# Kernel optimization log

Measured on AMD Instinct MI355X. Metric: run time of the kernel, lower is better.

The kernel has to match this reference:

```python
import jax, jax.numpy as jnp
import numpy as np

B, I, H = 16384, 512, 512
HH = H // 2


def _lrelu(v):
    return jnp.where(v > 0, v, 0.01 * v)


def setup_inputs() -> dict:
    key = jax.random.key(0)
    ks = jax.random.split(key, 20)
    s = 1.0 / np.sqrt(H)
    rn = lambda k, shp, sc: (jax.random.normal(k, shp, jnp.float32) * sc)
    return {
        "x": rn(ks[0], (B, I), 1.0),
        "h0": rn(ks[1], (1, B, H), 1.0),
        "c0": rn(ks[2], (1, B, H), 1.0),
        "cum": jax.random.uniform(ks[3], (B, 1), jnp.float32),
        # LSTM params (torch gate order i, f, g, o)
        "W_ih": rn(ks[4], (4 * H, I), s),
        "W_hh": rn(ks[5], (4 * H, H), s),
        "b_ih": rn(ks[6], (4 * H,), s),
        "b_hh": rn(ks[7], (4 * H,), s),
        # skip gate MLP
        "W_sp": rn(ks[8], (HH, H), s),
        "b_sp": rn(ks[9], (HH,), s),
        "W_sc": rn(ks[10], (HH, H), s),
        "b_sc": rn(ks[11], (HH,), s),
        "W_so": rn(ks[12], (1, HH), s),
        "b_so": rn(ks[13], (1,), s),
        # threshold gate MLP
        "W_tp": rn(ks[14], (HH, H), s),
        "b_tp": rn(ks[15], (HH,), s),
        "W_to": rn(ks[16], (1, HH), s),
        "b_to": rn(ks[17], (1,), s),
    }


def reference(x, h0, c0, cum, W_ih, W_hh, b_ih, b_hh,
              W_sp, b_sp, W_sc, b_sc, W_so, b_so,
              W_tp, b_tp, W_to, b_to):
    # single-step, single-layer LSTM
    gates = x @ W_ih.T + b_ih + h0[0] @ W_hh.T + b_hh  # [B, 4H]
    i_g, f_g, g_g, o_g = jnp.split(gates, 4, axis=-1)
    i_g = jax.nn.sigmoid(i_g)
    f_g = jax.nn.sigmoid(f_g)
    g_g = jnp.tanh(g_g)
    o_g = jax.nn.sigmoid(o_g)
    c1l = f_g * c0[0] + i_g * g_g          # [B, H]
    h1l = o_g * jnp.tanh(c1l)              # [B, H]
    h1, c1 = h1l[None], c1l[None]          # [1, B, H]

    # skip gate: delta prob from c0[-1], c1[-1]
    sg = _lrelu(c0[-1] @ W_sp.T + b_sp + c1[-1] @ W_sc.T + b_sc)  # [B, H/2]
    update_prob_delta = jax.nn.sigmoid(sg @ W_so.T + b_so)        # [B, 1]

    # threshold gate from c0[-1]
    tg = _lrelu(c0[-1] @ W_tp.T + b_tp)                           # [B, H/2]
    update_threshold = jax.nn.sigmoid(tg @ W_to.T + b_to)         # [B, 1]

    update_prob = cum + jnp.minimum(update_prob_delta, 1.0 - cum)  # [B, 1]
    # straight-through round: fwd hard threshold, bwd identity to prob
    hard = (update_prob > update_threshold).astype(jnp.float32)
    update_gate = update_prob + jax.lax.stop_gradient(hard - update_prob)

    new_h = update_gate * h1 + (1.0 - update_gate) * h0  # [1, B, H]
    new_c = update_gate * c1 + (1.0 - update_gate) * c0  # [1, B, H]
    update_cum = (1.0 - update_gate) * update_prob        # [B, 1]
    return (new_h, new_c, update_cum, update_prob_delta, update_prob)
```

## Files before the change

kernel.cpp:

```cpp
#include <hip/hip_runtime.h>
#include <math.h>

#define BB 16384
#define HH 512

typedef short short8 __attribute__((ext_vector_type(8)));
typedef float f32x4 __attribute__((ext_vector_type(4)));
typedef unsigned short ushort_t;

__device__ __forceinline__ float sigm(float v){ return 1.0f/(1.0f+expf(-v)); }

__device__ __forceinline__ unsigned short f2bf(float f){
    unsigned int u = __float_as_uint(f);
    u = u + 0x7FFFu + ((u>>16)&1u);
    return (unsigned short)(u>>16);
}
__device__ __forceinline__ float bf2f(unsigned short h){
    return __uint_as_float(((unsigned int)h)<<16);
}
__device__ __forceinline__ void gll16(const void* g, void* l){
    __builtin_amdgcn_global_load_lds((const __attribute__((address_space(1))) void*)g,
                                     (__attribute__((address_space(3))) void*)l, 16, 0, 0);
}
__device__ __forceinline__ void split_store(float v, ushort_t* ph, ushort_t* pl, int j){
    unsigned short h = f2bf(v);
    unsigned short l = f2bf(v - bf2f(h));
    ph[j] = h; pl[j] = l;
}

__global__ void k_prep_all(
    const float* __restrict__ x, const float* __restrict__ h0, const float* __restrict__ c0,
    const float* __restrict__ W_ih, const float* __restrict__ W_hh,
    const float* __restrict__ b_ih, const float* __restrict__ b_hh,
    const float* __restrict__ W_sp, const float* __restrict__ W_sc, const float* __restrict__ W_tp,
    const float* __restrict__ b_sp, const float* __restrict__ b_sc, const float* __restrict__ b_tp,
    ushort_t* __restrict__ A1h, ushort_t* __restrict__ A1l,
    ushort_t* __restrict__ A2h, ushort_t* __restrict__ A2l,
    ushort_t* __restrict__ B1h, ushort_t* __restrict__ B1l,
    ushort_t* __restrict__ B2h, ushort_t* __restrict__ B2l,
    float* __restrict__ bgp, float* __restrict__ bs2)
{
    int bid = blockIdx.x;
    if (bid < 8192) {
        int u = bid*256 + threadIdx.x;
        int r  = u & 255;
        int c  = (u >> 8) & 3;
        int kt = (u >> 10) & 31;
        int tm = u >> 15;
        int row = tm*256 + r;
        int k0 = kt*32 + c*8;
        const float* src = (k0 < 512) ? (x + (size_t)row*512 + k0)
                                      : (h0 + (size_t)row*512 + (k0-512));
        float4 v0 = *(const float4*)(src);
        float4 v1 = *(const float4*)(src+4);
        float vv[8] = {v0.x,v0.y,v0.z,v0.w,v1.x,v1.y,v1.z,v1.w};
        size_t off = (size_t)u * 8;
#pragma unroll
        for (int j=0;j<8;++j) split_store(vv[j], A1h+off, A1l+off, j);
    } else if (bid < 12288) {
        int u = (bid-8192)*256 + threadIdx.x;
        int r  = u & 127;
        int c  = (u >> 7) & 3;
        int tk = (u >> 9) & 15;
        int tm = u >> 13;
        int row = tm*128 + r;
        int k0 = tk*32 + c*8;
        const float* src = c0 + (size_t)row*512 + k0;
        float4 v0 = *(const float4*)(src);
        float4 v1 = *(const float4*)(src+4);
        float vv[8] = {v0.x,v0.y,v0.z,v0.w,v1.x,v1.y,v1.z,v1.w};
        size_t off = ((size_t)tm*32 + tk)*4096 + (size_t)(c*128 + r)*8;
#pragma unroll
        for (int j=0;j<8;++j) split_store(vv[j], A2h+off, A2l+off, j);
    } else if (bid < 13312) {
        int u = (bid-12288)*256 + threadIdx.x;
        int r  = u & 255;
        int c  = (u >> 8) & 3;
        int kt = (u >> 10) & 31;
        int tn = u >> 15;
        int g = (r>>4)&3;
        int h = tn*64 + (r>>6)*16 + (r&15);
        int wrow = g*512 + h;
        int k0 = kt*32 + c*8;
        const float* src = (k0 < 512) ? (W_ih + (size_t)wrow*512 + k0)
                                      : (W_hh + (size_t)wrow*512 + (k0-512));
        float4 v0 = *(const float4*)(src);
        float4 v1 = *(const float4*)(src+4);
        float vv[8] = {v0.x,v0.y,v0.z,v0.w,v1.x,v1.y,v1.z,v1.w};
        size_t off = (size_t)u * 8;
#pragma unroll
        for (int j=0;j<8;++j) split_store(vv[j], B1h+off, B1l+off, j);
        if (kt == 0 && c == 0) bgp[tn*256 + r] = b_ih[wrow] + b_hh[wrow];
    } else {
        int u = (bid-13312)*256 + threadIdx.x;
        int r  = u & 127;
        int c  = (u >> 7) & 3;
        int tk = (u >> 9) & 31;
        int tn = u >> 14;
        int n = tn*128 + r;
        int k0 = tk*32 + c*8;
        float vv[8];
        if (n < 256) {
            const float* src = (k0 < 512) ? (W_sp + (size_t)n*512 + k0)
                                          : (W_sc + (size_t)n*512 + (k0-512));
            float4 v0 = *(const float4*)(src);
            float4 v1 = *(const float4*)(src+4);
            vv[0]=v0.x; vv[1]=v0.y; vv[2]=v0.z; vv[3]=v0.w;
            vv[4]=v1.x; vv[5]=v1.y; vv[6]=v1.z; vv[7]=v1.w;
        } else if (k0 < 512) {
            const float* src = W_tp + (size_t)(n-256)*512 + k0;
            float4 v0 = *(const float4*)(src);
            float4 v1 = *(const float4*)(src+4);
            vv[0]=v0.x; vv[1]=v0.y; vv[2]=v0.z; vv[3]=v0.w;
            vv[4]=v1.x; vv[5]=v1.y; vv[6]=v1.z; vv[7]=v1.w;
        } else {
#pragma unroll
            for (int j=0;j<8;++j) vv[j] = 0.0f;
        }
        size_t off = (size_t)u * 8;
#pragma unroll
        for (int j=0;j<8;++j) split_store(vv[j], B2h+off, B2l+off, j);
        if (tk == 0 && c == 0) bs2[n] = (n < 256) ? (b_sp[n] + b_sc[n]) : b_tp[n-256];
    }
}

#define GSTEP(T, CA, CB, NA, NB, DO_READS, DO_STAGE, VMASM)                          \
  {                                                                                  \
    if (DO_READS) {                                                                  \
        const ushort_t* bufA1 = &lds[((T)+1) & 3][0];                                \
        const ushort_t* bufB1 = &lds[((T)+1) & 3][8192];                             \
        _Pragma("unroll") for (int f = 0; f < 8; ++f)                                \
            NA[f] = *(const short8*)&bufA1[aoff[f]];                                 \
        _Pragma("unroll") for (int f = 0; f < 4; ++f)                                \
            NB[f] = *(const short8*)&bufB1[boff[f]];                                 \
    }                                                                                \
    if (DO_STAGE) {                                                                  \
        const int uu = (T) + 3;                                                      \
        const ushort_t* As_ = ((uu >> 5) == 1) ? Al : Ah;                            \
        const ushort_t* Bs_ = ((uu >> 5) == 2) ? Bl : Bh;                            \
        size_t ga = ((size_t)tm*32 + (uu & 31))*8192 + (size_t)tid*8;                \
        size_t gb = ((size_t)tn*32 + (uu & 31))*8192 + (size_t)tid*8;                \
        ushort_t* dA = &lds[uu & 3][0];                                              \
        ushort_t* dB = &lds[uu & 3][8192];                                           \
        gll16(As_ + ga,        dA + tid*8);                                          \
        gll16(As_ + ga + 4096, dA + 4096 + tid*8);                                   \
        gll16(Bs_ + gb,        dB + tid*8);                                          \
        gll16(Bs_ + gb + 4096, dB + 4096 + tid*8);                                   \
    }                                                                                \
    _Pragma("unroll") for (int fm = 0; fm < 8; ++fm)                                 \
        _Pragma("unroll") for (int fn = 0; fn < 4; ++fn)                             \
            acc[fm][fn] = __builtin_amdgcn_mfma_f32_16x16x32_bf16(CA[fm], CB[fn], acc[fm][fn], 0,0,0); \
    VMASM;                                                                           \
    asm volatile("s_barrier" ::: "memory");                                          \
  }

__global__ __launch_bounds__(512, 2) void k_gemm_gates(
    const ushort_t* __restrict__ Ah, const ushort_t* __restrict__ Al,
    const ushort_t* __restrict__ Bh, const ushort_t* __restrict__ Bl,
    const float* __restrict__ bgp, const float* __restrict__ c0,
    float* __restrict__ outH, float* __restrict__ outC,
    ushort_t* __restrict__ A2h, ushort_t* __restrict__ A2l)
{
    __shared__ __align__(16) ushort_t lds[4][16384];
    const int tid  = threadIdx.x;
    const int lane = tid & 63;
    const int wid  = tid >> 6;
    const int wr   = wid >> 2;
    const int wc   = wid & 3;
    const int l15  = lane & 15;
    const int lq   = lane >> 4;
    const int bid  = (int)blockIdx.x;
    const int v    = (bid & 7)*64 + (bid >> 3);
    const int tm   = v >> 3;
    const int tn   = v & 7;

    f32x4 acc[8][4];
#pragma unroll
    for (int fn = 0; fn < 4; ++fn) {
        float bv = bgp[tn*256 + wc*64 + fn*16 + l15];
#pragma unroll
        for (int fm = 0; fm < 8; ++fm) {
            acc[fm][fn][0]=bv; acc[fm][fn][1]=bv; acc[fm][fn][2]=bv; acc[fm][fn][3]=bv;
        }
    }

    int aoff[8], boff[4];
#pragma unroll
    for (int f = 0; f < 8; ++f) aoff[f] = (lq*256 + wr*128 + f*16 + l15) * 8;
#pragma unroll
    for (int f = 0; f < 4; ++f) boff[f] = (lq*256 + wc*64 + f*16 + l15) * 8;

    short8 a0[8], b0[4], a1[8], b1[4];

#pragma unroll
    for (int u0 = 0; u0 < 3; ++u0) {
        size_t ga = ((size_t)tm*32 + u0)*8192 + (size_t)tid*8;
        size_t gb = ((size_t)tn*32 + u0)*8192 + (size_t)tid*8;
        gll16(Ah + ga,        &lds[u0][0]     + tid*8);
        gll16(Ah + ga + 4096, &lds[u0][4096]  + tid*8);
        gll16(Bh + gb,        &lds[u0][8192]  + tid*8);
        gll16(Bh + gb + 4096, &lds[u0][12288] + tid*8);
    }
    asm volatile("s_waitcnt vmcnt(4)" ::: "memory");
    asm volatile("s_barrier" ::: "memory");
#pragma unroll
    for (int f = 0; f < 8; ++f) a0[f] = *(const short8*)&lds[0][aoff[f]];
#pragma unroll
    for (int f = 0; f < 4; ++f) b0[f] = *(const short8*)&lds[0][8192 + boff[f]];

    for (int t = 0; t < 92; t += 2) {
        GSTEP(t,   a0, b0, a1, b1, 1, 1, asm volatile("s_waitcnt vmcnt(4)" ::: "memory"));
        GSTEP(t+1, a1, b1, a0, b0, 1, 1, asm volatile("s_waitcnt vmcnt(4)" ::: "memory"));
    }
    GSTEP(92, a0, b0, a1, b1, 1, 1, asm volatile("s_waitcnt vmcnt(4)" ::: "memory"));
    GSTEP(93, a1, b1, a0, b0, 1, 0, asm volatile("s_waitcnt vmcnt(0)" ::: "memory"));
    GSTEP(94, a0, b0, a1, b1, 1, 0, ((void)0));
    GSTEP(95, a1, b1, a0, b0, 0, 0, ((void)0));

    const int h = tn*64 + wc*16 + l15;
#pragma unroll
    for (int fm = 0; fm < 8; ++fm) {
        int row0 = tm*256 + wr*128 + fm*16 + lq*4;
#pragma unroll
        for (int r = 0; r < 4; ++r) {
            int row = row0 + r;
            size_t idx = (size_t)row*512 + h;
            float ig = sigm(acc[fm][0][r]);
            float fg = sigm(acc[fm][1][r]);
            float gg = tanhf(acc[fm][2][r]);
            float og = sigm(acc[fm][3][r]);
            float c1 = fg*c0[idx] + ig*gg;
            float h1 = og*tanhf(c1);
            outC[idx] = c1;
            outH[idx] = h1;
            unsigned short ch = f2bf(c1);
            unsigned short cl = f2bf(c1 - bf2f(ch));
            size_t a2 = ((size_t)(row>>7)*32 + 16 + (h>>5))*4096
                      + (size_t)((((h>>3)&3))*128 + (row&127))*8 + (h&7);
            A2h[a2] = ch;
            A2l[a2] = cl;
        }
    }
}

#define SSTEP(T, CA, CB, NA, NB, DO_READS, DO_STAGE, VMASM)                          \
  {                                                                                  \
    if (DO_READS) {                                                                  \
        const ushort_t* bufA1 = &lds2[((T)+1) & 3][0];                               \
        const ushort_t* bufB1 = &lds2[((T)+1) & 3][4096];                            \
        _Pragma("unroll") for (int f = 0; f < 4; ++f)                                \
            NA[f] = *(const short8*)&bufA1[aoff[f]];                                 \
        _Pragma("unroll") for (int f = 0; f < 4; ++f)                                \
            NB[f] = *(const short8*)&bufB1[boff[f]];                                 \
    }                                                                                \
    if (DO_STAGE) {                                                                  \
        const int uu = (T) + 3;                                                      \
        const ushort_t* As_ = ((uu >> 5) == 1) ? Al : Ah;                            \
        const ushort_t* Bs_ = ((uu >> 5) == 2) ? Bl : Bh;                            \
        size_t ga = ((size_t)tm*32 + (uu & 31))*4096 + (size_t)tid*8;                \
        size_t gb = ((size_t)tn*32 + (uu & 31))*4096 + (size_t)tid*8;                \
        ushort_t* dA = &lds2[uu & 3][0];                                             \
        ushort_t* dB = &lds2[uu & 3][4096];                                          \
        gll16(As_ + ga,        dA + tid*8);                                          \
        gll16(As_ + ga + 2048, dA + 2048 + tid*8);                                   \
        gll16(Bs_ + gb,        dB + tid*8);                                          \
        gll16(Bs_ + gb + 2048, dB + 2048 + tid*8);                                   \
    }                                                                                \
    _Pragma("unroll") for (int fm = 0; fm < 4; ++fm)                                 \
        _Pragma("unroll") for (int fn = 0; fn < 4; ++fn)                             \
            acc[fm][fn] = __builtin_amdgcn_mfma_f32_16x16x32_bf16(CA[fm], CB[fn], acc[fm][fn], 0,0,0); \
    VMASM;                                                                           \
    asm volatile("s_barrier" ::: "memory");                                          \
  }

__global__ __launch_bounds__(256, 2) void k_gemm_sgtg(
    const ushort_t* __restrict__ Ah, const ushort_t* __restrict__ Al,
    const ushort_t* __restrict__ Bh, const ushort_t* __restrict__ Bl,
    const float* __restrict__ bs2,
    float* __restrict__ sgtg)
{
    __shared__ __align__(16) ushort_t lds2[4][8192];
    const int tid  = threadIdx.x;
    const int lane = tid & 63;
    const int wid  = tid >> 6;
    const int wr   = wid >> 1;
    const int wc   = wid & 1;
    const int l15  = lane & 15;
    const int lq   = lane >> 4;
    const int bid  = (int)blockIdx.x;
    const int v    = (bid & 7)*64 + (bid >> 3);
    const int tm   = v >> 2;
    const int tn   = v & 3;

    f32x4 acc[4][4];
#pragma unroll
    for (int fn = 0; fn < 4; ++fn) {
        float bv = bs2[tn*128 + wc*64 + fn*16 + l15];
#pragma unroll
        for (int fm = 0; fm < 4; ++fm) {
            acc[fm][fn][0]=bv; acc[fm][fn][1]=bv; acc[fm][fn][2]=bv; acc[fm][fn][3]=bv;
        }
    }

    int aoff[4], boff[4];
#pragma unroll
    for (int f = 0; f < 4; ++f) {
        aoff[f] = (lq*128 + wr*64 + f*16 + l15) * 8;
        boff[f] = (lq*128 + wc*64 + f*16 + l15) * 8;
    }

    short8 a0[4], b0[4], a1[4], b1[4];

#pragma unroll
    for (int u0 = 0; u0 < 3; ++u0) {
        size_t ga = ((size_t)tm*32 + u0)*4096 + (size_t)tid*8;
        size_t gb = ((size_t)tn*32 + u0)*4096 + (size_t)tid*8;
        gll16(Ah + ga,        &lds2[u0][0]    + tid*8);
        gll16(Ah + ga + 2048, &lds2[u0][2048] + tid*8);
        gll16(Bh + gb,        &lds2[u0][4096] + tid*8);
        gll16(Bh + gb + 2048, &lds2[u0][6144] + tid*8);
    }
    asm volatile("s_waitcnt vmcnt(4)" ::: "memory");
    asm volatile("s_barrier" ::: "memory");
#pragma unroll
    for (int f = 0; f < 4; ++f) a0[f] = *(const short8*)&lds2[0][aoff[f]];
#pragma unroll
    for (int f = 0; f < 4; ++f) b0[f] = *(const short8*)&lds2[0][4096 + boff[f]];

    for (int t = 0; t < 92; t += 2) {
        SSTEP(t,   a0, b0, a1, b1, 1, 1, asm volatile("s_waitcnt vmcnt(4)" ::: "memory"));
        SSTEP(t+1, a1, b1, a0, b0, 1, 1, asm volatile("s_waitcnt vmcnt(4)" ::: "memory"));
    }
    SSTEP(92, a0, b0, a1, b1, 1, 1, asm volatile("s_waitcnt vmcnt(4)" ::: "memory"));
    SSTEP(93, a1, b1, a0, b0, 1, 0, asm volatile("s_waitcnt vmcnt(0)" ::: "memory"));
    SSTEP(94, a0, b0, a1, b1, 1, 0, ((void)0));
    SSTEP(95, a1, b1, a0, b0, 0, 0, ((void)0));

#pragma unroll
    for (int fm = 0; fm < 4; ++fm) {
        int row0 = tm*128 + wr*64 + fm*16 + lq*4;
#pragma unroll
        for (int fn = 0; fn < 4; ++fn) {
            int n = tn*128 + wc*64 + fn*16 + l15;
#pragma unroll
            for (int r = 0; r < 4; ++r) {
                int row = row0 + r;
                float vv = acc[fm][fn][r];
                vv = vv > 0.f ? vv : 0.01f*vv;
                sgtg[(size_t)row*512 + n] = vv;
            }
        }
    }
}

__global__ __launch_bounds__(256) void k_final(
    const float* __restrict__ sgtg,
    const float* __restrict__ h0, const float* __restrict__ c0,
    const float* __restrict__ cum,
    const float* __restrict__ W_so, const float* __restrict__ b_so,
    const float* __restrict__ W_to, const float* __restrict__ b_to,
    float* __restrict__ outH, float* __restrict__ outC,
    float* __restrict__ outCum, float* __restrict__ outDelta, float* __restrict__ outProb)
{
    int w = threadIdx.x >> 6;
    int lane = threadIdx.x & 63;
    int b = blockIdx.x * 4 + w;
    const float* row = sgtg + (size_t)b * 512;
    float so = 0.f, to = 0.f;
#pragma unroll
    for (int u = 0; u < 4; ++u) {
        int c = lane + 64 * u;
        so = fmaf(row[c], W_so[c], so);
        to = fmaf(row[256 + c], W_to[c], to);
    }
#pragma unroll
    for (int off = 32; off; off >>= 1) {
        so += __shfl_down(so, off);
        to += __shfl_down(to, off);
    }
    so = __shfl(so, 0);
    to = __shfl(to, 0);
    float delta = sigm(so + b_so[0]);
    float thr   = sigm(to + b_to[0]);
    float cu = cum[b];
    float prob = cu + fminf(delta, 1.0f - cu);
    float hard = (prob > thr) ? 1.0f : 0.0f;
    if (lane == 0) {
        outDelta[b] = delta;
        outProb[b]  = prob;
        outCum[b]   = (1.0f - hard) * prob;
    }
    if (hard == 0.0f) {
#pragma unroll
        for (int u = 0; u < 8; ++u) {
            size_t idx = (size_t)b * 512 + lane + 64 * u;
            outH[idx] = h0[idx];
            outC[idx] = c0[idx];
        }
    }
}

extern "C" void kernel_launch(void* const* d_in, const int* in_sizes, int n_in,
                              void* d_out, int out_size, void* d_ws, size_t ws_size,
                              hipStream_t stream)
{
    const float* x    = (const float*)d_in[0];
    const float* h0   = (const float*)d_in[1];
    const float* c0   = (const float*)d_in[2];
    const float* cum  = (const float*)d_in[3];
    const float* W_ih = (const float*)d_in[4];
    const float* W_hh = (const float*)d_in[5];
    const float* b_ih = (const float*)d_in[6];
    const float* b_hh = (const float*)d_in[7];
    const float* W_sp = (const float*)d_in[8];
    const float* b_sp = (const float*)d_in[9];
    const float* W_sc = (const float*)d_in[10];
    const float* b_sc = (const float*)d_in[11];
    const float* W_so = (const float*)d_in[12];
    const float* b_so = (const float*)d_in[13];
    const float* W_tp = (const float*)d_in[14];
    const float* b_tp = (const float*)d_in[15];
    const float* W_to = (const float*)d_in[16];
    const float* b_to = (const float*)d_in[17];

    float* out      = (float*)d_out;
    float* outH     = out;
    float* outC     = out + (size_t)BB * HH;
    float* outCum   = out + (size_t)2 * BB * HH;
    float* outDelta = outCum + BB;
    float* outProb  = outDelta + BB;

    char* w = (char*)d_ws;
    ushort_t* A1h = (ushort_t*)(w);
    ushort_t* A1l = (ushort_t*)(w + 33554432ull);
    ushort_t* A2h = (ushort_t*)(w + 67108864ull);
    ushort_t* A2l = (ushort_t*)(w + 100663296ull);
    ushort_t* B1h = (ushort_t*)(w + 134217728ull);
    ushort_t* B1l = (ushort_t*)(w + 138412032ull);
    ushort_t* B2h = (ushort_t*)(w + 142606336ull);
    ushort_t* B2l = (ushort_t*)(w + 143654912ull);
    float*    bgp = (float*)(w + 144703488ull);
    float*    bs2 = (float*)(w + 144711680ull);
    float*    sgtg = (float*)A1h;

    k_prep_all<<<13568, 256, 0, stream>>>(x, h0, c0, W_ih, W_hh, b_ih, b_hh,
                                          W_sp, W_sc, W_tp, b_sp, b_sc, b_tp,
                                          A1h, A1l, A2h, A2l, B1h, B1l, B2h, B2l,
                                          bgp, bs2);
    k_gemm_gates<<<512, 512, 0, stream>>>(A1h, A1l, B1h, B1l, bgp, c0,
                                          outH, outC, A2h, A2l);
    k_gemm_sgtg<<<512, 256, 0, stream>>>(A2h, A2l, B2h, B2l, bs2, sgtg);
    k_final<<<4096, 256, 0, stream>>>(sgtg, h0, c0, cum, W_so, b_so, W_to, b_to,
                                      outH, outC, outCum, outDelta, outProb);
}
```

Baseline: 333.1 us.

## Fuse c0 split into gates epilogue and output-projection dot into sgtg GEMM

```diff
diff --git a/kernel.cpp b/kernel.cpp
--- a/kernel.cpp
+++ b/kernel.cpp
@@ -29,16 +29,16 @@
 }
 
 __global__ void k_prep_all(
-    const float* __restrict__ x, const float* __restrict__ h0, const float* __restrict__ c0,
+    const float* __restrict__ x, const float* __restrict__ h0,
     const float* __restrict__ W_ih, const float* __restrict__ W_hh,
     const float* __restrict__ b_ih, const float* __restrict__ b_hh,
     const float* __restrict__ W_sp, const float* __restrict__ W_sc, const float* __restrict__ W_tp,
     const float* __restrict__ b_sp, const float* __restrict__ b_sc, const float* __restrict__ b_tp,
     ushort_t* __restrict__ A1h, ushort_t* __restrict__ A1l,
-    ushort_t* __restrict__ A2h, ushort_t* __restrict__ A2l,
     ushort_t* __restrict__ B1h, ushort_t* __restrict__ B1l,
     ushort_t* __restrict__ B2h, ushort_t* __restrict__ B2l,
-    float* __restrict__ bgp, float* __restrict__ bs2)
+    float* __restrict__ bgp, float* __restrict__ bs2,
+    float* __restrict__ so, float* __restrict__ to)
 {
     int bid = blockIdx.x;
     if (bid < 8192) {
@@ -57,23 +57,8 @@
         size_t off = (size_t)u * 8;
 #pragma unroll
         for (int j=0;j<8;++j) split_store(vv[j], A1h+off, A1l+off, j);
-    } else if (bid < 12288) {
+    } else if (bid < 9216) {
         int u = (bid-8192)*256 + threadIdx.x;
-        int r  = u & 127;
-        int c  = (u >> 7) & 3;
-        int tk = (u >> 9) & 15;
-        int tm = u >> 13;
-        int row = tm*128 + r;
-        int k0 = tk*32 + c*8;
-        const float* src = c0 + (size_t)row*512 + k0;
-        float4 v0 = *(const float4*)(src);
-        float4 v1 = *(const float4*)(src+4);
-        float vv[8] = {v0.x,v0.y,v0.z,v0.w,v1.x,v1.y,v1.z,v1.w};
-        size_t off = ((size_t)tm*32 + tk)*4096 + (size_t)(c*128 + r)*8;
-#pragma unroll
-        for (int j=0;j<8;++j) split_store(vv[j], A2h+off, A2l+off, j);
-    } else if (bid < 13312) {
-        int u = (bid-12288)*256 + threadIdx.x;
         int r  = u & 255;
         int c  = (u >> 8) & 3;
         int kt = (u >> 10) & 31;
@@ -91,8 +76,8 @@
 #pragma unroll
         for (int j=0;j<8;++j) split_store(vv[j], B1h+off, B1l+off, j);
         if (kt == 0 && c == 0) bgp[tn*256 + r] = b_ih[wrow] + b_hh[wrow];
-    } else {
-        int u = (bid-13312)*256 + threadIdx.x;
+    } else if (bid < 9472) {
+        int u = (bid-9216)*256 + threadIdx.x;
         int r  = u & 127;
         int c  = (u >> 7) & 3;
         int tk = (u >> 9) & 31;
@@ -121,6 +106,10 @@
 #pragma unroll
         for (int j=0;j<8;++j) split_store(vv[j], B2h+off, B2l+off, j);
         if (tk == 0 && c == 0) bs2[n] = (n < 256) ? (b_sp[n] + b_sc[n]) : b_tp[n-256];
+    } else {
+        int idx = (bid-9472)*256 + threadIdx.x;
+        so[idx] = 0.0f;
+        to[idx] = 0.0f;
     }
 }
 
@@ -225,20 +214,27 @@
         for (int r = 0; r < 4; ++r) {
             int row = row0 + r;
             size_t idx = (size_t)row*512 + h;
+            float c0v = c0[idx];
             float ig = sigm(acc[fm][0][r]);
             float fg = sigm(acc[fm][1][r]);
             float gg = tanhf(acc[fm][2][r]);
             float og = sigm(acc[fm][3][r]);
-            float c1 = fg*c0[idx] + ig*gg;
+            float c1 = fg*c0v + ig*gg;
             float h1 = og*tanhf(c1);
             outC[idx] = c1;
             outH[idx] = h1;
+            size_t a2base = (size_t)((((h>>3)&3))*128 + (row&127))*8 + (h&7);
+            size_t tmrow  = (size_t)(row>>7)*32;
             unsigned short ch = f2bf(c1);
             unsigned short cl = f2bf(c1 - bf2f(ch));
-            size_t a2 = ((size_t)(row>>7)*32 + 16 + (h>>5))*4096
-                      + (size_t)((((h>>3)&3))*128 + (row&127))*8 + (h&7);
-            A2h[a2] = ch;
-            A2l[a2] = cl;
+            size_t a2hi = (tmrow + 16 + (h>>5))*4096 + a2base;
+            A2h[a2hi] = ch;
+            A2l[a2hi] = cl;
+            unsigned short zh = f2bf(c0v);
+            unsigned short zl = f2bf(c0v - bf2f(zh));
+            size_t a2lo = (tmrow + (h>>5))*4096 + a2base;
+            A2h[a2lo] = zh;
+            A2l[a2lo] = zl;
         }
     }
 }
@@ -277,7 +273,8 @@
     const ushort_t* __restrict__ Ah, const ushort_t* __restrict__ Al,
     const ushort_t* __restrict__ Bh, const ushort_t* __restrict__ Bl,
     const float* __restrict__ bs2,
-    float* __restrict__ sgtg)
+    const float* __restrict__ W_so, const float* __restrict__ W_to,
+    float* __restrict__ so, float* __restrict__ to)
 {
     __shared__ __align__(16) ushort_t lds2[4][8192];
     const int tid  = threadIdx.x;
@@ -336,52 +333,43 @@
     SSTEP(94, a0, b0, a1, b1, 1, 0, ((void)0));
     SSTEP(95, a1, b1, a0, b0, 0, 0, ((void)0));
 
+    const float* Wv = (tn < 2) ? W_so : W_to;
+    float* dst = (tn < 2) ? so : to;
 #pragma unroll
     for (int fm = 0; fm < 4; ++fm) {
-        int row0 = tm*128 + wr*64 + fm*16 + lq*4;
-#pragma unroll
-        for (int fn = 0; fn < 4; ++fn) {
-            int n = tn*128 + wc*64 + fn*16 + l15;
-#pragma unroll
-            for (int r = 0; r < 4; ++r) {
-                int row = row0 + r;
+#pragma unroll
+        for (int r = 0; r < 4; ++r) {
+            int row = tm*128 + wr*64 + fm*16 + lq*4 + r;
+            float p = 0.0f;
+#pragma unroll
+            for (int fn = 0; fn < 4; ++fn) {
+                int n = tn*128 + wc*64 + fn*16 + l15;
                 float vv = acc[fm][fn][r];
                 vv = vv > 0.f ? vv : 0.01f*vv;
-                sgtg[(size_t)row*512 + n] = vv;
+                p = fmaf(vv, Wv[n & 255], p);
             }
-        }
-    }
-}
-
-__global__ __launch_bounds__(256) void k_final(
-    const float* __restrict__ sgtg,
+            p += __shfl_xor(p, 1);
+            p += __shfl_xor(p, 2);
+            p += __shfl_xor(p, 4);
+            p += __shfl_xor(p, 8);
+            if (l15 == 0) atomicAdd(&dst[row], p);
+        }
+    }
+}
+
+__global__ __launch_bounds__(256) void k_final2(
+    const float* __restrict__ so, const float* __restrict__ to,
+    const float* __restrict__ cum,
+    const float* __restrict__ b_so, const float* __restrict__ b_to,
     const float* __restrict__ h0, const float* __restrict__ c0,
-    const float* __restrict__ cum,
-    const float* __restrict__ W_so, const float* __restrict__ b_so,
-    const float* __restrict__ W_to, const float* __restrict__ b_to,
     float* __restrict__ outH, float* __restrict__ outC,
     float* __restrict__ outCum, float* __restrict__ outDelta, float* __restrict__ outProb)
 {
     int w = threadIdx.x >> 6;
     int lane = threadIdx.x & 63;
     int b = blockIdx.x * 4 + w;
-    const float* row = sgtg + (size_t)b * 512;
-    float so = 0.f, to = 0.f;
-#pragma unroll
-    for (int u = 0; u < 4; ++u) {
-        int c = lane + 64 * u;
-        so = fmaf(row[c], W_so[c], so);
-        to = fmaf(row[256 + c], W_to[c], to);
-    }
-#pragma unroll
-    for (int off = 32; off; off >>= 1) {
-        so += __shfl_down(so, off);
-        to += __shfl_down(to, off);
-    }
-    so = __shfl(so, 0);
-    to = __shfl(to, 0);
-    float delta = sigm(so + b_so[0]);
-    float thr   = sigm(to + b_to[0]);
+    float delta = sigm(so[b] + b_so[0]);
+    float thr   = sigm(to[b] + b_to[0]);
     float cu = cum[b];
     float prob = cu + fminf(delta, 1.0f - cu);
     float hard = (prob > thr) ? 1.0f : 0.0f;
@@ -441,15 +429,17 @@
     ushort_t* B2l = (ushort_t*)(w + 143654912ull);
     float*    bgp = (float*)(w + 144703488ull);
     float*    bs2 = (float*)(w + 144711680ull);
-    float*    sgtg = (float*)A1h;
-
-    k_prep_all<<<13568, 256, 0, stream>>>(x, h0, c0, W_ih, W_hh, b_ih, b_hh,
-                                          W_sp, W_sc, W_tp, b_sp, b_sc, b_tp,
-                                          A1h, A1l, A2h, A2l, B1h, B1l, B2h, B2l,
-                                          bgp, bs2);
+    float*    so  = (float*)(w + 144713728ull);
+    float*    to  = (float*)(w + 144779264ull);
+
+    k_prep_all<<<9536, 256, 0, stream>>>(x, h0, W_ih, W_hh, b_ih, b_hh,
+                                         W_sp, W_sc, W_tp, b_sp, b_sc, b_tp,
+                                         A1h, A1l, B1h, B1l, B2h, B2l,
+                                         bgp, bs2, so, to);
     k_gemm_gates<<<512, 512, 0, stream>>>(A1h, A1l, B1h, B1l, bgp, c0,
                                           outH, outC, A2h, A2l);
-    k_gemm_sgtg<<<512, 256, 0, stream>>>(A2h, A2l, B2h, B2l, bs2, sgtg);
-    k_final<<<4096, 256, 0, stream>>>(sgtg, h0, c0, cum, W_so, b_so, W_to, b_to,
-                                      outH, outC, outCum, outDelta, outProb);
-}
+    k_gemm_sgtg<<<512, 256, 0, stream>>>(A2h, A2l, B2h, B2l, bs2,
+                                         W_so, W_to, so, to);
+    k_final2<<<4096, 256, 0, stream>>>(so, to, cum, b_so, b_to, h0, c0,
+                                       outH, outC, outCum, outDelta, outProb);
+}
```

New measurement: 334.3 us. About the same (+0.4%).

## Fuse final gate reduction and blend into sgtg GEMM epilogue with atomics

Applied to the files above, without the earlier changes.

```diff
diff --git a/kernel.cpp b/kernel.cpp
--- a/kernel.cpp
+++ b/kernel.cpp
@@ -38,7 +38,8 @@
     ushort_t* __restrict__ A2h, ushort_t* __restrict__ A2l,
     ushort_t* __restrict__ B1h, ushort_t* __restrict__ B1l,
     ushort_t* __restrict__ B2h, ushort_t* __restrict__ B2l,
-    float* __restrict__ bgp, float* __restrict__ bs2)
+    float* __restrict__ bgp, float* __restrict__ bs2,
+    float* __restrict__ so, float* __restrict__ to, int* __restrict__ cnt)
 {
     int bid = blockIdx.x;
     if (bid < 8192) {
@@ -91,7 +92,7 @@
 #pragma unroll
         for (int j=0;j<8;++j) split_store(vv[j], B1h+off, B1l+off, j);
         if (kt == 0 && c == 0) bgp[tn*256 + r] = b_ih[wrow] + b_hh[wrow];
-    } else {
+    } else if (bid < 13568) {
         int u = (bid-13312)*256 + threadIdx.x;
         int r  = u & 127;
         int c  = (u >> 7) & 3;
@@ -121,6 +122,11 @@
 #pragma unroll
         for (int j=0;j<8;++j) split_store(vv[j], B2h+off, B2l+off, j);
         if (tk == 0 && c == 0) bs2[n] = (n < 256) ? (b_sp[n] + b_sc[n]) : b_tp[n-256];
+    } else {
+        int idx = (bid-13568)*256 + threadIdx.x;
+        so[idx] = 0.0f;
+        to[idx] = 0.0f;
+        if (idx < 128) cnt[idx] = 0;
     }
 }
 
@@ -277,9 +283,16 @@
     const ushort_t* __restrict__ Ah, const ushort_t* __restrict__ Al,
     const ushort_t* __restrict__ Bh, const ushort_t* __restrict__ Bl,
     const float* __restrict__ bs2,
-    float* __restrict__ sgtg)
+    const float* __restrict__ W_so, const float* __restrict__ W_to,
+    float* __restrict__ so, float* __restrict__ to, int* __restrict__ cnt,
+    const float* __restrict__ cum,
+    const float* __restrict__ b_so, const float* __restrict__ b_to,
+    const float* __restrict__ h0, const float* __restrict__ c0,
+    float* __restrict__ outH, float* __restrict__ outC,
+    float* __restrict__ outCum, float* __restrict__ outDelta, float* __restrict__ outProb)
 {
     __shared__ __align__(16) ushort_t lds2[4][8192];
+    __shared__ int lastFlag;
     const int tid  = threadIdx.x;
     const int lane = tid & 63;
     const int wid  = tid >> 6;
@@ -336,66 +349,60 @@
     SSTEP(94, a0, b0, a1, b1, 1, 0, ((void)0));
     SSTEP(95, a1, b1, a0, b0, 0, 0, ((void)0));
 
+    const float* Wv = (tn < 2) ? W_so : W_to;
+    float* dst = (tn < 2) ? so : to;
 #pragma unroll
     for (int fm = 0; fm < 4; ++fm) {
-        int row0 = tm*128 + wr*64 + fm*16 + lq*4;
-#pragma unroll
-        for (int fn = 0; fn < 4; ++fn) {
-            int n = tn*128 + wc*64 + fn*16 + l15;
-#pragma unroll
-            for (int r = 0; r < 4; ++r) {
-                int row = row0 + r;
+#pragma unroll
+        for (int r = 0; r < 4; ++r) {
+            int row = tm*128 + wr*64 + fm*16 + lq*4 + r;
+            float p = 0.0f;
+#pragma unroll
+            for (int fn = 0; fn < 4; ++fn) {
+                int n = tn*128 + wc*64 + fn*16 + l15;
                 float vv = acc[fm][fn][r];
                 vv = vv > 0.f ? vv : 0.01f*vv;
-                sgtg[(size_t)row*512 + n] = vv;
+                p = fmaf(vv, Wv[n & 255], p);
             }
-        }
-    }
-}
-
-__global__ __launch_bounds__(256) void k_final(
-    const float* __restrict__ sgtg,
-    const float* __restrict__ h0, const float* __restrict__ c0,
-    const float* __restrict__ cum,
-    const float* __restrict__ W_so, const float* __restrict__ b_so,
-    const float* __restrict__ W_to, const float* __restrict__ b_to,
-    float* __restrict__ outH, float* __restrict__ outC,
-    float* __restrict__ outCum, float* __restrict__ outDelta, float* __restrict__ outProb)
-{
-    int w = threadIdx.x >> 6;
-    int lane = threadIdx.x & 63;
-    int b = blockIdx.x * 4 + w;
-    const float* row = sgtg + (size_t)b * 512;
-    float so = 0.f, to = 0.f;
-#pragma unroll
-    for (int u = 0; u < 4; ++u) {
-        int c = lane + 64 * u;
-        so = fmaf(row[c], W_so[c], so);
-        to = fmaf(row[256 + c], W_to[c], to);
-    }
-#pragma unroll
-    for (int off = 32; off; off >>= 1) {
-        so += __shfl_down(so, off);
-        to += __shfl_down(to, off);
-    }
-    so = __shfl(so, 0);
-    to = __shfl(to, 0);
-    float delta = sigm(so + b_so[0]);
-    float thr   = sigm(to + b_to[0]);
-    float cu = cum[b];
-    float prob = cu + fminf(delta, 1.0f - cu);
-    float hard = (prob > thr) ? 1.0f : 0.0f;
-    if (lane == 0) {
-        outDelta[b] = delta;
-        outProb[b]  = prob;
-        outCum[b]   = (1.0f - hard) * prob;
-    }
-    if (hard == 0.0f) {
-#pragma unroll
-        for (int u = 0; u < 8; ++u) {
-            size_t idx = (size_t)b * 512 + lane + 64 * u;
-            outH[idx] = h0[idx];
-            outC[idx] = c0[idx];
+            p += __shfl_xor(p, 1);
+            p += __shfl_xor(p, 2);
+            p += __shfl_xor(p, 4);
+            p += __shfl_xor(p, 8);
+            if (l15 == 0) atomicAdd(&dst[row], p);
+        }
+    }
+
+    __threadfence();
+    if (tid == 0) {
+        int old = atomicAdd(&cnt[tm], 1);
+        lastFlag = (old == 3) ? 1 : 0;
+    }
+    __syncthreads();
+    if (lastFlag) {
+        __threadfence();
+        int rr   = tid >> 1;
+        int half = tid & 1;
+        int b = tm*128 + rr;
+        float delta = sigm(so[b] + b_so[0]);
+        float thr   = sigm(to[b] + b_to[0]);
+        float cu = cum[b];
+        float prob = cu + fminf(delta, 1.0f - cu);
+        float hard = (prob > thr) ? 1.0f : 0.0f;
+        if (half == 0) {
+            outDelta[b] = delta;
+            outProb[b]  = prob;
+            outCum[b]   = (1.0f - hard) * prob;
+        }
+        if (hard == 0.0f) {
+            const float4* src_h = (const float4*)(h0 + (size_t)b*512 + half*256);
+            const float4* src_c = (const float4*)(c0 + (size_t)b*512 + half*256);
+            float4* dst_h = (float4*)(outH + (size_t)b*512 + half*256);
+            float4* dst_c = (float4*)(outC + (size_t)b*512 + half*256);
+#pragma unroll
+            for (int u = 0; u < 64; ++u) {
+                dst_h[u] = src_h[u];
+                dst_c[u] = src_c[u];
+            }
         }
     }
 }
@@ -441,15 +448,18 @@
     ushort_t* B2l = (ushort_t*)(w + 143654912ull);
     float*    bgp = (float*)(w + 144703488ull);
     float*    bs2 = (float*)(w + 144711680ull);
-    float*    sgtg = (float*)A1h;
-
-    k_prep_all<<<13568, 256, 0, stream>>>(x, h0, c0, W_ih, W_hh, b_ih, b_hh,
+    float*    so  = (float*)(w + 144713728ull);
+    float*    to  = (float*)(w + 144779264ull);
+    int*      cnt = (int*)(w + 144844800ull);
+
+    k_prep_all<<<13632, 256, 0, stream>>>(x, h0, c0, W_ih, W_hh, b_ih, b_hh,
                                           W_sp, W_sc, W_tp, b_sp, b_sc, b_tp,
                                           A1h, A1l, A2h, A2l, B1h, B1l, B2h, B2l,
-                                          bgp, bs2);
+                                          bgp, bs2, so, to, cnt);
     k_gemm_gates<<<512, 512, 0, stream>>>(A1h, A1l, B1h, B1l, bgp, c0,
                                           outH, outC, A2h, A2l);
-    k_gemm_sgtg<<<512, 256, 0, stream>>>(A2h, A2l, B2h, B2l, bs2, sgtg);
-    k_final<<<4096, 256, 0, stream>>>(sgtg, h0, c0, cum, W_so, b_so, W_to, b_to,
-                                      outH, outC, outCum, outDelta, outProb);
-}
+    k_gemm_sgtg<<<512, 256, 0, stream>>>(A2h, A2l, B2h, B2l, bs2,
+                                         W_so, W_to, so, to, cnt,
+                                         cum, b_so, b_to, h0, c0,
+                                         outH, outC, outCum, outDelta, outProb);
+}
```

Result: slower. 375.9 us (+12.8%).

## Use 4-wave blocks with 128x128 per-wave tiles in gates GEMM

Applied to the files above, without the earlier changes.

```diff
diff --git a/kernel.cpp b/kernel.cpp
--- a/kernel.cpp
+++ b/kernel.cpp
@@ -131,30 +131,30 @@
         const ushort_t* bufB1 = &lds[((T)+1) & 3][8192];                             \
         _Pragma("unroll") for (int f = 0; f < 8; ++f)                                \
             NA[f] = *(const short8*)&bufA1[aoff[f]];                                 \
-        _Pragma("unroll") for (int f = 0; f < 4; ++f)                                \
+        _Pragma("unroll") for (int f = 0; f < 8; ++f)                                \
             NB[f] = *(const short8*)&bufB1[boff[f]];                                 \
     }                                                                                \
     if (DO_STAGE) {                                                                  \
         const int uu = (T) + 3;                                                      \
         const ushort_t* As_ = ((uu >> 5) == 1) ? Al : Ah;                            \
         const ushort_t* Bs_ = ((uu >> 5) == 2) ? Bl : Bh;                            \
-        size_t ga = ((size_t)tm*32 + (uu & 31))*8192 + (size_t)tid*8;                \
-        size_t gb = ((size_t)tn*32 + (uu & 31))*8192 + (size_t)tid*8;                \
+        const ushort_t* gA = As_ + ((size_t)tm*32 + (uu & 31))*8192;                 \
+        const ushort_t* gB = Bs_ + ((size_t)tn*32 + (uu & 31))*8192;                 \
         ushort_t* dA = &lds[uu & 3][0];                                              \
         ushort_t* dB = &lds[uu & 3][8192];                                           \
-        gll16(As_ + ga,        dA + tid*8);                                          \
-        gll16(As_ + ga + 4096, dA + 4096 + tid*8);                                   \
-        gll16(Bs_ + gb,        dB + tid*8);                                          \
-        gll16(Bs_ + gb + 4096, dB + 4096 + tid*8);                                   \
+        _Pragma("unroll") for (int q = 0; q < 4; ++q)                                \
+            gll16(gA + q*2048 + (size_t)tid*8, dA + q*2048 + tid*8);                 \
+        _Pragma("unroll") for (int q = 0; q < 4; ++q)                                \
+            gll16(gB + q*2048 + (size_t)tid*8, dB + q*2048 + tid*8);                 \
     }                                                                                \
     _Pragma("unroll") for (int fm = 0; fm < 8; ++fm)                                 \
-        _Pragma("unroll") for (int fn = 0; fn < 4; ++fn)                             \
+        _Pragma("unroll") for (int fn = 0; fn < 8; ++fn)                             \
             acc[fm][fn] = __builtin_amdgcn_mfma_f32_16x16x32_bf16(CA[fm], CB[fn], acc[fm][fn], 0,0,0); \
     VMASM;                                                                           \
     asm volatile("s_barrier" ::: "memory");                                          \
   }
 
-__global__ __launch_bounds__(512, 2) void k_gemm_gates(
+__global__ __launch_bounds__(256, 1) void k_gemm_gates(
     const ushort_t* __restrict__ Ah, const ushort_t* __restrict__ Al,
     const ushort_t* __restrict__ Bh, const ushort_t* __restrict__ Bl,
     const float* __restrict__ bgp, const float* __restrict__ c0,
@@ -165,8 +165,8 @@
     const int tid  = threadIdx.x;
     const int lane = tid & 63;
     const int wid  = tid >> 6;
-    const int wr   = wid >> 2;
-    const int wc   = wid & 3;
+    const int wr   = wid >> 1;
+    const int wc   = wid & 1;
     const int l15  = lane & 15;
     const int lq   = lane >> 4;
     const int bid  = (int)blockIdx.x;
@@ -174,71 +174,77 @@
     const int tm   = v >> 3;
     const int tn   = v & 7;
 
-    f32x4 acc[8][4];
-#pragma unroll
-    for (int fn = 0; fn < 4; ++fn) {
-        float bv = bgp[tn*256 + wc*64 + fn*16 + l15];
+    f32x4 acc[8][8];
+#pragma unroll
+    for (int fn = 0; fn < 8; ++fn) {
+        float bv = bgp[tn*256 + wc*128 + fn*16 + l15];
 #pragma unroll
         for (int fm = 0; fm < 8; ++fm) {
             acc[fm][fn][0]=bv; acc[fm][fn][1]=bv; acc[fm][fn][2]=bv; acc[fm][fn][3]=bv;
         }
     }
 
-    int aoff[8], boff[4];
-#pragma unroll
-    for (int f = 0; f < 8; ++f) aoff[f] = (lq*256 + wr*128 + f*16 + l15) * 8;
-#pragma unroll
-    for (int f = 0; f < 4; ++f) boff[f] = (lq*256 + wc*64 + f*16 + l15) * 8;
-
-    short8 a0[8], b0[4], a1[8], b1[4];
+    int aoff[8], boff[8];
+#pragma unroll
+    for (int f = 0; f < 8; ++f) {
+        aoff[f] = (lq*256 + wr*128 + f*16 + l15) * 8;
+        boff[f] = (lq*256 + wc*128 + f*16 + l15) * 8;
+    }
+
+    short8 a0[8], b0[8], a1[8], b1[8];
 
 #pragma unroll
     for (int u0 = 0; u0 < 3; ++u0) {
-        size_t ga = ((size_t)tm*32 + u0)*8192 + (size_t)tid*8;
-        size_t gb = ((size_t)tn*32 + u0)*8192 + (size_t)tid*8;
-        gll16(Ah + ga,        &lds[u0][0]     + tid*8);
-        gll16(Ah + ga + 4096, &lds[u0][4096]  + tid*8);
-        gll16(Bh + gb,        &lds[u0][8192]  + tid*8);
-        gll16(Bh + gb + 4096, &lds[u0][12288] + tid*8);
-    }
-    asm volatile("s_waitcnt vmcnt(4)" ::: "memory");
+        const ushort_t* gA = Ah + ((size_t)tm*32 + u0)*8192;
+        const ushort_t* gB = Bh + ((size_t)tn*32 + u0)*8192;
+#pragma unroll
+        for (int q = 0; q < 4; ++q)
+            gll16(gA + q*2048 + (size_t)tid*8, &lds[u0][q*2048 + tid*8]);
+#pragma unroll
+        for (int q = 0; q < 4; ++q)
+            gll16(gB + q*2048 + (size_t)tid*8, &lds[u0][8192 + q*2048 + tid*8]);
+    }
+    asm volatile("s_waitcnt vmcnt(8)" ::: "memory");
     asm volatile("s_barrier" ::: "memory");
 #pragma unroll
     for (int f = 0; f < 8; ++f) a0[f] = *(const short8*)&lds[0][aoff[f]];
 #pragma unroll
-    for (int f = 0; f < 4; ++f) b0[f] = *(const short8*)&lds[0][8192 + boff[f]];
+    for (int f = 0; f < 8; ++f) b0[f] = *(const short8*)&lds[0][8192 + boff[f]];
 
     for (int t = 0; t < 92; t += 2) {
-        GSTEP(t,   a0, b0, a1, b1, 1, 1, asm volatile("s_waitcnt vmcnt(4)" ::: "memory"));
-        GSTEP(t+1, a1, b1, a0, b0, 1, 1, asm volatile("s_waitcnt vmcnt(4)" ::: "memory"));
-    }
-    GSTEP(92, a0, b0, a1, b1, 1, 1, asm volatile("s_waitcnt vmcnt(4)" ::: "memory"));
+        GSTEP(t,   a0, b0, a1, b1, 1, 1, asm volatile("s_waitcnt vmcnt(8)" ::: "memory"));
+        GSTEP(t+1, a1, b1, a0, b0, 1, 1, asm volatile("s_waitcnt vmcnt(8)" ::: "memory"));
+    }
+    GSTEP(92, a0, b0, a1, b1, 1, 1, asm volatile("s_waitcnt vmcnt(8)" ::: "memory"));
     GSTEP(93, a1, b1, a0, b0, 1, 0, asm volatile("s_waitcnt vmcnt(0)" ::: "memory"));
     GSTEP(94, a0, b0, a1, b1, 1, 0, ((void)0));
     GSTEP(95, a1, b1, a0, b0, 0, 0, ((void)0));
 
-    const int h = tn*64 + wc*16 + l15;
 #pragma unroll
     for (int fm = 0; fm < 8; ++fm) {
         int row0 = tm*256 + wr*128 + fm*16 + lq*4;
 #pragma unroll
-        for (int r = 0; r < 4; ++r) {
-            int row = row0 + r;
-            size_t idx = (size_t)row*512 + h;
-            float ig = sigm(acc[fm][0][r]);
-            float fg = sigm(acc[fm][1][r]);
-            float gg = tanhf(acc[fm][2][r]);
-            float og = sigm(acc[fm][3][r]);
-            float c1 = fg*c0[idx] + ig*gg;
-            float h1 = og*tanhf(c1);
-            outC[idx] = c1;
-            outH[idx] = h1;
-            unsigned short ch = f2bf(c1);
-            unsigned short cl = f2bf(c1 - bf2f(ch));
-            size_t a2 = ((size_t)(row>>7)*32 + 16 + (h>>5))*4096
-                      + (size_t)((((h>>3)&3))*128 + (row&127))*8 + (h&7);
-            A2h[a2] = ch;
-            A2l[a2] = cl;
+        for (int hg = 0; hg < 2; ++hg) {
+            int h = tn*64 + (wc*2 + hg)*16 + l15;
+#pragma unroll
+            for (int r = 0; r < 4; ++r) {
+                int row = row0 + r;
+                size_t idx = (size_t)row*512 + h;
+                float ig = sigm(acc[fm][hg*4+0][r]);
+                float fg = sigm(acc[fm][hg*4+1][r]);
+                float gg = tanhf(acc[fm][hg*4+2][r]);
+                float og = sigm(acc[fm][hg*4+3][r]);
+                float c1 = fg*c0[idx] + ig*gg;
+                float h1 = og*tanhf(c1);
+                outC[idx] = c1;
+                outH[idx] = h1;
+                unsigned short ch = f2bf(c1);
+                unsigned short cl = f2bf(c1 - bf2f(ch));
+                size_t a2 = ((size_t)(row>>7)*32 + 16 + (h>>5))*4096
+                          + (size_t)((((h>>3)&3))*128 + (row&127))*8 + (h&7);
+                A2h[a2] = ch;
+                A2l[a2] = cl;
+            }
         }
     }
 }
@@ -447,7 +453,7 @@
                                           W_sp, W_sc, W_tp, b_sp, b_sc, b_tp,
                                           A1h, A1l, A2h, A2l, B1h, B1l, B2h, B2l,
                                           bgp, bs2);
-    k_gemm_gates<<<512, 512, 0, stream>>>(A1h, A1l, B1h, B1l, bgp, c0,
+    k_gemm_gates<<<512, 256, 0, stream>>>(A1h, A1l, B1h, B1l, bgp, c0,
                                           outH, outC, A2h, A2l);
     k_gemm_sgtg<<<512, 256, 0, stream>>>(A2h, A2l, B2h, B2l, bs2, sgtg);
     k_final<<<4096, 256, 0, stream>>>(sgtg, h0, c0, cum, W_so, b_so, W_to, b_to,
```

Result: slower. 412.7 us (+23.9%).
